# Performance work log

Measured on AMD Instinct MI355X. Metric: run time of the kernel, lower is better.

Reference implementation:

```python
import jax, jax.numpy as jnp
import numpy as np

N_NODES, FEAT, EMB, BATCH, NUM_SAMPLE = 100000, 256, 256, 10000, 32


def setup_inputs() -> dict:
    key = jax.random.key(0)
    ks = jax.random.split(key, 8)
    sc = 1.0 / np.sqrt(FEAT).astype(np.float32)
    return {
        "nodes": jax.random.randint(ks[0], (BATCH,), 0, N_NODES),
        "neigh_idx": jax.random.randint(ks[1], (BATCH, NUM_SAMPLE), 0, N_NODES),
        "id2feat": jax.random.normal(ks[2], (N_NODES, FEAT), jnp.float32),
        "Wq": jax.random.normal(ks[3], (FEAT, EMB), jnp.float32) * sc,
        "bq": jnp.zeros((EMB,), jnp.float32),
        "Wk": jax.random.normal(ks[4], (FEAT, EMB), jnp.float32) * sc,
        "bk": jnp.zeros((EMB,), jnp.float32),
        "Wv": jax.random.normal(ks[5], (FEAT, EMB), jnp.float32) * sc,
        "bv": jnp.zeros((EMB,), jnp.float32),
    }


def reference(nodes, neigh_idx, id2feat, Wq, bq, Wk, bk, Wv, bv):
    # Gather: self feats [B, F] and sampled neighbor feats [B, S, F]
    self_feats = id2feat[nodes]
    neigh_feats = id2feat[neigh_idx]
    S = neigh_idx.shape[1]
    # Keys/values over [neighbors, self] -> [B, S+1, F]
    cat = jnp.concatenate([neigh_feats, self_feats[:, None, :]], axis=1)
    Q = self_feats @ Wq + bq               # [B, E]
    K = cat @ Wk + bk                       # [B, S+1, E]
    V = cat @ Wv + bv                       # [B, S+1, E]
    scores = jnp.einsum('be,bse->bs', Q, K)  # [B, S+1]
    # Faithful to original mask loop: with full neighbor lists, columns >= num_sample
    # (the appended self key) are masked out.
    mask = jnp.arange(S + 1) >= S
    scores = jnp.where(mask[None, :], -jnp.inf, scores)
    attn = jax.nn.softmax(scores, axis=-1)   # [B, S+1]
    return jnp.einsum('bs,bse->be', attn, V)  # [B, E]
```

## Files before the change

kernel.cpp:

```cpp
#include <hip/hip_runtime.h>
#include <math.h>

#define F 256
#define E 256
#define S 32

__global__ __launch_bounds__(256) void prep_M(const float* __restrict__ Wq,
                                              const float* __restrict__ bq,
                                              const float* __restrict__ Wk,
                                              float* __restrict__ M,
                                              float* __restrict__ c) {
    const int i = blockIdx.x;
    const int j = threadIdx.x;
    __shared__ float row[E];
    row[j] = (i < F) ? Wq[i * E + j] : bq[j];
    __syncthreads();
    float acc = 0.f;
#pragma unroll 8
    for (int e = 0; e < E; e += 4) {
        float4 w = *reinterpret_cast<const float4*>(&Wk[j * E + e]);
        acc += row[e] * w.x + row[e + 1] * w.y + row[e + 2] * w.z + row[e + 3] * w.w;
    }
    if (i < F) M[i * F + j] = acc;
    else       c[j] = acc;
}

__global__ __launch_bounds__(256) void gemm_bias(const float* __restrict__ X,
                                                 const int* __restrict__ idx,
                                                 const float* __restrict__ W,
                                                 const float* __restrict__ bias,
                                                 float* __restrict__ out,
                                                 int rows) {
    __shared__ float xsT[64][68];
    __shared__ float wt[64][64];
    const int tid = threadIdx.x;
    const int tx = tid & 15, ty = tid >> 4;
    const int bn = blockIdx.x, bm = blockIdx.y;
    const int jb = bn * 64 + tx * 4;
    float acc[4][4] = {{0.f}};

    for (int k0 = 0; k0 < F; k0 += 64) {
#pragma unroll
        for (int p = 0; p < 4; ++p) {
            const int lr = p * 16 + ty;
            const int lk = tx * 4;
            const int gr = bm * 64 + lr;
            const int grc = gr < rows ? gr : rows - 1;
            const long grow = idx ? (long)idx[grc] : (long)grc;
            float4 v = *reinterpret_cast<const float4*>(&X[grow * F + k0 + lk]);
            xsT[lk + 0][lr] = v.x; xsT[lk + 1][lr] = v.y;
            xsT[lk + 2][lr] = v.z; xsT[lk + 3][lr] = v.w;
            const int wk = p * 16 + ty;
            float4 wv = *reinterpret_cast<const float4*>(&W[(size_t)(k0 + wk) * E + bn * 64 + tx * 4]);
            *reinterpret_cast<float4*>(&wt[wk][tx * 4]) = wv;
        }
        __syncthreads();
#pragma unroll 16
        for (int k = 0; k < 64; ++k) {
            float4 a = *reinterpret_cast<const float4*>(&xsT[k][ty * 4]);
            float4 b = *reinterpret_cast<const float4*>(&wt[k][tx * 4]);
            acc[0][0] += a.x * b.x; acc[0][1] += a.x * b.y; acc[0][2] += a.x * b.z; acc[0][3] += a.x * b.w;
            acc[1][0] += a.y * b.x; acc[1][1] += a.y * b.y; acc[1][2] += a.y * b.z; acc[1][3] += a.y * b.w;
            acc[2][0] += a.z * b.x; acc[2][1] += a.z * b.y; acc[2][2] += a.z * b.z; acc[2][3] += a.z * b.w;
            acc[3][0] += a.w * b.x; acc[3][1] += a.w * b.y; acc[3][2] += a.w * b.z; acc[3][3] += a.w * b.w;
        }
        __syncthreads();
    }

    const float4 bb = *reinterpret_cast<const float4*>(&bias[jb]);
#pragma unroll
    for (int v = 0; v < 4; ++v) {
        const int r = bm * 64 + ty * 4 + v;
        if (r < rows) {
            float4 o;
            o.x = acc[v][0] + bb.x; o.y = acc[v][1] + bb.y;
            o.z = acc[v][2] + bb.z; o.w = acc[v][3] + bb.w;
            *reinterpret_cast<float4*>(&out[(size_t)r * E + jb]) = o;
        }
    }
}

__global__ __launch_bounds__(256) void attn_gather(const int* __restrict__ neigh_idx,
                                                   const float* __restrict__ id2feat,
                                                   float* __restrict__ qtm,
                                                   int B) {
    const int node = blockIdx.x * 4 + (threadIdx.x >> 6);
    const int lane = threadIdx.x & 63;
    if (node >= B) return;

    const int idxv = neigh_idx[node * S + (lane & (S - 1))];
    const float4 qv = *reinterpret_cast<const float4*>(&qtm[(size_t)node * F + lane * 4]);

    float4 rows[S];
#pragma unroll
    for (int s = 0; s < S; ++s) {
        const int nid = __builtin_amdgcn_readlane(idxv, s);
        rows[s] = *reinterpret_cast<const float4*>(&id2feat[(size_t)nid * F + lane * 4]);
    }

    float ps[S];
#pragma unroll
    for (int s = 0; s < S; ++s) {
        float p = rows[s].x * qv.x + rows[s].y * qv.y + rows[s].z * qv.z + rows[s].w * qv.w;
#pragma unroll
        for (int off = 32; off; off >>= 1) p += __shfl_xor(p, off);
        ps[s] = p;
    }

    float mx = ps[0];
#pragma unroll
    for (int s = 1; s < S; ++s) mx = fmaxf(mx, ps[s]);
    float sum = 0.f;
#pragma unroll
    for (int s = 0; s < S; ++s) { ps[s] = __expf(ps[s] - mx); sum += ps[s]; }
    const float inv = 1.0f / sum;

    float4 acc = make_float4(0.f, 0.f, 0.f, 0.f);
#pragma unroll
    for (int s = 0; s < S; ++s) {
        const float w = ps[s] * inv;
        acc.x += w * rows[s].x; acc.y += w * rows[s].y;
        acc.z += w * rows[s].z; acc.w += w * rows[s].w;
    }
    *reinterpret_cast<float4*>(&qtm[(size_t)node * F + lane * 4]) = acc;
}

extern "C" void kernel_launch(void* const* d_in, const int* in_sizes, int n_in,
                              void* d_out, int out_size, void* d_ws, size_t ws_size,
                              hipStream_t stream) {
    const int*   nodes   = (const int*)d_in[0];
    const int*   neigh   = (const int*)d_in[1];
    const float* id2feat = (const float*)d_in[2];
    const float* Wq      = (const float*)d_in[3];
    const float* bq      = (const float*)d_in[4];
    const float* Wk      = (const float*)d_in[5];
    const float* Wv      = (const float*)d_in[7];
    const float* bv      = (const float*)d_in[8];
    float* out = (float*)d_out;
    const int B = in_sizes[0];

    float* Mbuf = (float*)d_ws;
    float* cbuf = Mbuf + F * F;
    float* qtm  = cbuf + F;

    prep_M<<<dim3(F + 1), dim3(256), 0, stream>>>(Wq, bq, Wk, Mbuf, cbuf);
    gemm_bias<<<dim3(4, (B + 63) / 64), dim3(256), 0, stream>>>(id2feat, nodes, Mbuf, cbuf, qtm, B);
    attn_gather<<<dim3((B + 3) / 4), dim3(256), 0, stream>>>(neigh, id2feat, qtm, B);
    gemm_bias<<<dim3(4, (B + 63) / 64), dim3(256), 0, stream>>>(qtm, nullptr, Wv, bv, out, B);
}
```

Before: 131.0 us.

## Stream neighbor rows with online softmax and double-buffered chunks

The attention kernel used to keep all 32 gathered neighbor rows in registers (128 VGPRs for the rows alone) before computing scores, the softmax and the weighted sum. It now loads rows in chunks of 4 into two alternating buffers and folds each chunk into a running max, sum and accumulator (online softmax). The aim is to cut register pressure so more waves fit per CU and gather latency is hidden better. In exchange it adds per-row branching and exp rescaling, and keeps fewer loads in flight per wave.

```diff
diff --git a/kernel.cpp b/kernel.cpp
--- a/kernel.cpp
+++ b/kernel.cpp
@@ -4,6 +4,7 @@
 #define F 256
 #define E 256
 #define S 32
+#define CH 4
 
 __global__ __launch_bounds__(256) void prep_M(const float* __restrict__ Wq,
                                               const float* __restrict__ bq,
@@ -80,6 +81,37 @@
     }
 }
 
+__device__ __forceinline__ void ld_chunk(float4* d, int idxv, int s0,
+                                         const float* __restrict__ t, int lane) {
+#pragma unroll
+    for (int j = 0; j < CH; ++j) {
+        const int nid = __builtin_amdgcn_readlane(idxv, s0 + j);
+        d[j] = *reinterpret_cast<const float4*>(&t[(size_t)nid * F + lane * 4]);
+    }
+}
+
+__device__ __forceinline__ void proc_chunk(const float4* v, const float4 qv,
+                                           float& m, float& l, float4& acc) {
+#pragma unroll
+    for (int j = 0; j < CH; ++j) {
+        float p = v[j].x * qv.x + v[j].y * qv.y + v[j].z * qv.z + v[j].w * qv.w;
+#pragma unroll
+        for (int off = 32; off; off >>= 1) p += __shfl_xor(p, off);
+        if (p <= m) {
+            const float w = __expf(p - m);
+            l += w;
+            acc.x += w * v[j].x; acc.y += w * v[j].y;
+            acc.z += w * v[j].z; acc.w += w * v[j].w;
+        } else {
+            const float c = __expf(m - p);
+            l = l * c + 1.f;
+            acc.x = acc.x * c + v[j].x; acc.y = acc.y * c + v[j].y;
+            acc.z = acc.z * c + v[j].z; acc.w = acc.w * c + v[j].w;
+            m = p;
+        }
+    }
+}
+
 __global__ __launch_bounds__(256) void attn_gather(const int* __restrict__ neigh_idx,
                                                    const float* __restrict__ id2feat,
                                                    float* __restrict__ qtm,
@@ -91,38 +123,31 @@
     const int idxv = neigh_idx[node * S + (lane & (S - 1))];
     const float4 qv = *reinterpret_cast<const float4*>(&qtm[(size_t)node * F + lane * 4]);
 
-    float4 rows[S];
-#pragma unroll
-    for (int s = 0; s < S; ++s) {
-        const int nid = __builtin_amdgcn_readlane(idxv, s);
-        rows[s] = *reinterpret_cast<const float4*>(&id2feat[(size_t)nid * F + lane * 4]);
-    }
+    float m = -INFINITY, l = 0.f;
+    float4 acc = make_float4(0.f, 0.f, 0.f, 0.f);
 
-    float ps[S];
-#pragma unroll
-    for (int s = 0; s < S; ++s) {
-        float p = rows[s].x * qv.x + rows[s].y * qv.y + rows[s].z * qv.z + rows[s].w * qv.w;
-#pragma unroll
-        for (int off = 32; off; off >>= 1) p += __shfl_xor(p, off);
-        ps[s] = p;
-    }
+    float4 va[CH], vb[CH];
+    ld_chunk(va, idxv, 0, id2feat, lane);
+    ld_chunk(vb, idxv, 4, id2feat, lane);
+    proc_chunk(va, qv, m, l, acc);
+    ld_chunk(va, idxv, 8, id2feat, lane);
+    proc_chunk(vb, qv, m, l, acc);
+    ld_chunk(vb, idxv, 12, id2feat, lane);
+    proc_chunk(va, qv, m, l, acc);
+    ld_chunk(va, idxv, 16, id2feat, lane);
+    proc_chunk(vb, qv, m, l, acc);
+    ld_chunk(vb, idxv, 20, id2feat, lane);
+    proc_chunk(va, qv, m, l, acc);
+    ld_chunk(va, idxv, 24, id2feat, lane);
+    proc_chunk(vb, qv, m, l, acc);
+    ld_chunk(vb, idxv, 28, id2feat, lane);
+    proc_chunk(va, qv, m, l, acc);
+    proc_chunk(vb, qv, m, l, acc);
 
-    float mx = ps[0];
-#pragma unroll
-    for (int s = 1; s < S; ++s) mx = fmaxf(mx, ps[s]);
-    float sum = 0.f;
-#pragma unroll
-    for (int s = 0; s < S; ++s) { ps[s] = __expf(ps[s] - mx); sum += ps[s]; }
-    const float inv = 1.0f / sum;
-
-    float4 acc = make_float4(0.f, 0.f, 0.f, 0.f);
-#pragma unroll
-    for (int s = 0; s < S; ++s) {
-        const float w = ps[s] * inv;
-        acc.x += w * rows[s].x; acc.y += w * rows[s].y;
-        acc.z += w * rows[s].z; acc.w += w * rows[s].w;
-    }
-    *reinterpret_cast<float4*>(&qtm[(size_t)node * F + lane * 4]) = acc;
+    const float inv = 1.0f / l;
+    float4 o;
+    o.x = acc.x * inv; o.y = acc.y * inv; o.z = acc.z * inv; o.w = acc.w * inv;
+    *reinterpret_cast<float4*>(&qtm[(size_t)node * F + lane * 4]) = o;
 }
 
 extern "C" void kernel_launch(void* const* d_in, const int* in_sizes, int n_in,
```

Result: slower. 134.7 us (+2.8%).
